# Optimization experiments

Measured on AMD Instinct MI355X. Metric: run time of the kernel, lower is better.

The kernel has to match this reference:

```python
import jax, jax.numpy as jnp
import numpy as np

D_MODEL = 1024
NUM_HEADS = 16
HEAD_DIM = D_MODEL // NUM_HEADS  # 64
THETA = 10000.0
B, S = 2, 2048


def setup_inputs() -> dict:
    key = jax.random.key(0)
    k1, k2, k3 = jax.random.split(key, 3)
    sigma_qkv = (2.0 / (D_MODEL + 3 * D_MODEL)) ** 0.5
    sigma_o = (2.0 / (D_MODEL + D_MODEL)) ** 0.5
    x = jax.random.normal(k1, (B, S, D_MODEL), dtype=jnp.float32)
    w_qkv = jax.random.normal(k2, (3 * D_MODEL, D_MODEL), dtype=jnp.float32) * sigma_qkv
    w_o = jax.random.normal(k3, (D_MODEL, D_MODEL), dtype=jnp.float32) * sigma_o
    token_positions = jnp.arange(S, dtype=jnp.int32)
    return {"x": x, "w_qkv": w_qkv, "w_o": w_o, "token_positions": token_positions, "mask": 1}


def _rope(t, pos):
    # t: (B, H, S, HEAD_DIM); pos: (S,) int
    ids = jnp.arange(HEAD_DIM // 2, dtype=jnp.float32)
    freqs = pos.astype(jnp.float32)[:, None] * (THETA ** (-2.0 * ids / HEAD_DIM))  # (S, HEAD_DIM/2)
    cos, sin = jnp.cos(freqs), jnp.sin(freqs)
    even, odd = t[..., 0::2], t[..., 1::2]
    r_even = even * cos - odd * sin
    r_odd = odd * cos + even * sin
    # interleave back to original layout
    return jnp.stack([r_even, r_odd], axis=-1).reshape(t.shape)


def reference(x, w_qkv, w_o, token_positions, mask):
    # fused QKV projection: Linear computes x @ W^T with W [out, in]
    qkv = x @ w_qkv.T  # (B, S, 3*D_MODEL)
    q, k, v = jnp.split(qkv, 3, axis=-1)

    def to_heads(t):
        return t.reshape(B, S, NUM_HEADS, HEAD_DIM).transpose(0, 2, 1, 3)  # (B, H, S, Dh)

    q, k, v = to_heads(q), to_heads(k), to_heads(v)
    q = _rope(q, token_positions)
    k = _rope(k, token_positions)

    scores = jnp.einsum('bhqd,bhkd->bhqk', q, k)
    if mask:  # causal: lower-triangular allowed
        causal = jnp.tril(jnp.ones((S, S), dtype=bool))
        scores = jnp.where(causal, scores, -jnp.inf)
    attn = jax.nn.softmax(scores * (HEAD_DIM ** -0.5), axis=-1)
    out = jnp.einsum('bhqk,bhkd->bhqd', attn, v)  # (B, H, S, Dh)
    out = out.transpose(0, 2, 1, 3).reshape(B, S, D_MODEL)
    return out @ w_o.T
```

## Files before the change

### kernel.cpp

```cpp
#include <hip/hip_runtime.h>
#include <hip/hip_bf16.h>
#include <math.h>

typedef __bf16 bf16_t;
typedef __bf16 bf16x8 __attribute__((ext_vector_type(8)));
typedef __bf16 bf16x4 __attribute__((ext_vector_type(4)));
typedef float  f32x4  __attribute__((ext_vector_type(4)));

#define D_MODEL 1024
#define NH      16
#define HD      64
#define BATCH   2
#define SEQ     2048
#define MROWS   (BATCH*SEQ)
#define QKVN    (3*D_MODEL)
#define FA_PAD  72
#define SCALE_LOG2E 0.18033688011112042f

__device__ __forceinline__ void async_cp16(const bf16_t* g, bf16_t* l) {
    __builtin_amdgcn_global_load_lds(
        (const __attribute__((address_space(1))) void*)g,
        (__attribute__((address_space(3))) void*)l,
        16, 0, 0);
}

__global__ void cvt_all(const float* __restrict__ x, const float* __restrict__ wq,
                        const float* __restrict__ wo,
                        bf16_t* __restrict__ xb, bf16_t* __restrict__ wqb,
                        bf16_t* __restrict__ wob) {
    const int nx = MROWS * D_MODEL, nq = QKVN * D_MODEL;
    int i = (blockIdx.x * blockDim.x + threadIdx.x) * 4;
    const float* s; bf16_t* d; int off;
    if (i < nx)           { s = x;  d = xb;  off = i; }
    else if (i < nx + nq) { s = wq; d = wqb; off = i - nx; }
    else                  { s = wo; d = wob; off = i - nx - nq; }
    float4 v = *(const float4*)(s + off);
    d[off]     = (bf16_t)v.x;
    d[off + 1] = (bf16_t)v.y;
    d[off + 2] = (bf16_t)v.z;
    d[off + 3] = (bf16_t)v.w;
}

template <typename OutT, int NI>
__global__ __launch_bounds__(256) void gemm_nt(const bf16_t* __restrict__ A,
                                               const bf16_t* __restrict__ Bm,
                                               OutT* __restrict__ C,
                                               int M, int N, int K) {
    __shared__ __align__(16) bf16_t As[128 * 32];
    __shared__ __align__(16) bf16_t Bs[NI * 32 * 32];
    const int tid  = threadIdx.x;
    const int w    = tid >> 6;
    const int lane = tid & 63;
    const int quad = lane >> 4;
    const int l16  = lane & 15;
    const int m0   = blockIdx.x * 128;
    const int n0   = blockIdx.y * (NI * 32);
    const int wm   = (w >> 1) * 64;
    const int wn   = (w & 1) * (NI * 16);

    f32x4 acc[4][NI];
    #pragma unroll
    for (int i = 0; i < 4; i++)
        #pragma unroll
        for (int j = 0; j < NI; j++)
            acc[i][j] = (f32x4){0.f, 0.f, 0.f, 0.f};

    const bf16_t* Ag0 = A  + (size_t)(m0 + (tid >> 2)) * K + (tid & 3) * 8;
    const bf16_t* Ag1 = Ag0 + (size_t)64 * K;
    const bf16_t* Bg0 = Bm + (size_t)(n0 + (tid >> 2)) * K + (tid & 3) * 8;
    const bf16_t* Bg1 = Bg0 + (size_t)64 * K;
    bf16_t* Al0 = &As[(size_t)tid * 8];
    bf16_t* Al1 = &As[((size_t)tid + 256) * 8];
    bf16_t* Bl0 = &Bs[(size_t)tid * 8];
    bf16_t* Bl1 = &Bs[((size_t)tid + 256) * 8];

    for (int k0 = 0; k0 < K; k0 += 32) {
        async_cp16(Ag0 + k0, Al0);
        async_cp16(Ag1 + k0, Al1);
        async_cp16(Bg0 + k0, Bl0);
        if (NI == 4) async_cp16(Bg1 + k0, Bl1);
        __syncthreads();

        bf16x8 af[4], bfr[NI];
        #pragma unroll
        for (int mi = 0; mi < 4; mi++)
            af[mi] = *(const bf16x8*)&As[(wm + mi * 16 + l16) * 32 + quad * 8];
        #pragma unroll
        for (int ni = 0; ni < NI; ni++)
            bfr[ni] = *(const bf16x8*)&Bs[(wn + ni * 16 + l16) * 32 + quad * 8];
        #pragma unroll
        for (int mi = 0; mi < 4; mi++)
            #pragma unroll
            for (int ni = 0; ni < NI; ni++)
                acc[mi][ni] = __builtin_amdgcn_mfma_f32_16x16x32_bf16(
                    af[mi], bfr[ni], acc[mi][ni], 0, 0, 0);
        __syncthreads();
    }

    #pragma unroll
    for (int mi = 0; mi < 4; mi++)
        #pragma unroll
        for (int ni = 0; ni < NI; ni++) {
            const int col = n0 + wn + ni * 16 + l16;
            #pragma unroll
            for (int r = 0; r < 4; r++) {
                const int row = m0 + wm + mi * 16 + quad * 4 + r;
                C[(size_t)row * N + col] = (OutT)acc[mi][ni][r];
            }
        }
}

__global__ __launch_bounds__(256) void rope_split(const bf16_t* __restrict__ qkv,
                                                  const int* __restrict__ pos,
                                                  bf16_t* __restrict__ Qh,
                                                  bf16_t* __restrict__ Kh,
                                                  bf16_t* __restrict__ VT) {
    __shared__ bf16_t vs[128][FA_PAD];
    const int tid   = threadIdx.x;
    const int s_loc = tid >> 1;
    const int half  = tid & 1;
    const int s0    = blockIdx.x * 128;
    const int bh    = blockIdx.y;
    const int b     = bh >> 4, h = bh & 15;
    const int s     = s0 + s_loc;

    const bf16_t* row = qkv + (size_t)(b * SEQ + s) * QKVN + h * HD + half * 32;

    bf16_t qbuf[32], kbuf[32], vbuf[32];
    #pragma unroll
    for (int j = 0; j < 4; j++) {
        *(bf16x8*)&qbuf[j * 8] = *(const bf16x8*)(row + j * 8);
        *(bf16x8*)&kbuf[j * 8] = *(const bf16x8*)(row + D_MODEL + j * 8);
        *(bf16x8*)&vbuf[j * 8] = *(const bf16x8*)(row + 2 * D_MODEL + j * 8);
    }

    const float pf = (float)pos[s];
    #pragma unroll
    for (int p = 0; p < 16; p++) {
        const int d2 = half * 16 + p;
        const float inv = __expf(-0.28782313662425575f * (float)d2);
        const float f = pf * inv;
        const float c = cosf(f), sn = sinf(f);
        float qe = (float)qbuf[2 * p], qo = (float)qbuf[2 * p + 1];
        float ke = (float)kbuf[2 * p], ko = (float)kbuf[2 * p + 1];
        qbuf[2 * p]     = (bf16_t)(qe * c - qo * sn);
        qbuf[2 * p + 1] = (bf16_t)(qo * c + qe * sn);
        kbuf[2 * p]     = (bf16_t)(ke * c - ko * sn);
        kbuf[2 * p + 1] = (bf16_t)(ko * c + ke * sn);
    }

    bf16_t* qdst = Qh + ((size_t)bh * SEQ + s) * HD + half * 32;
    bf16_t* kdst = Kh + ((size_t)bh * SEQ + s) * HD + half * 32;
    #pragma unroll
    for (int j = 0; j < 4; j++) {
        *(bf16x8*)(qdst + j * 8) = *(bf16x8*)&qbuf[j * 8];
        *(bf16x8*)(kdst + j * 8) = *(bf16x8*)&kbuf[j * 8];
        *(bf16x8*)&vs[s_loc][half * 32 + j * 8] = *(bf16x8*)&vbuf[j * 8];
    }
    __syncthreads();

    const int d  = tid >> 2;
    const int sc = tid & 3;
    bf16_t tmp[32];
    #pragma unroll
    for (int i = 0; i < 32; i++) tmp[i] = vs[sc * 32 + i][d];
    bf16_t* vdst = VT + ((size_t)bh * HD + d) * SEQ + s0 + sc * 32;
    #pragma unroll
    for (int j = 0; j < 4; j++)
        *(bf16x8*)(vdst + j * 8) = *(bf16x8*)&tmp[j * 8];
}

__global__ __launch_bounds__(256) void flash_attn(const bf16_t* __restrict__ Qh,
                                                  const bf16_t* __restrict__ Kh,
                                                  const bf16_t* __restrict__ VT,
                                                  bf16_t* __restrict__ AO) {
    __shared__ __align__(16) bf16_t Ks[64 * FA_PAD];
    __shared__ __align__(16) bf16_t Vs[64 * FA_PAD];
    __shared__ __align__(16) bf16_t pT[4][16][FA_PAD];

    const int tid  = threadIdx.x;
    const int w    = tid >> 6;
    const int lane = tid & 63;
    const int quad = lane >> 4;
    const int l16  = lane & 15;

    const int bid = blockIdx.x;
    const int xcd = bid & 7;
    const int mm  = bid >> 3;
    const int bh  = (mm >> 5) * 8 + xcd;
    const int qt  = 31 - (mm & 31);

    const bf16_t* Qb = Qh + (size_t)bh * SEQ * HD;
    const bf16_t* Kb = Kh + (size_t)bh * SEQ * HD;
    const bf16_t* Vb = VT + (size_t)bh * HD * SEQ;

    const int q0 = qt * 64 + w * 16;
    const bf16x8 aq0 = *(const bf16x8*)(Qb + (size_t)(q0 + l16) * HD + quad * 8);
    const bf16x8 aq1 = *(const bf16x8*)(Qb + (size_t)(q0 + l16) * HD + 32 + quad * 8);

    const int srow0 = tid >> 3, scol = (tid & 7) * 8;
    const int lds_off0 = srow0 * FA_PAD + scol;
    const int lds_off1 = (srow0 + 32) * FA_PAD + scol;

    f32x4 o[4];
    #pragma unroll
    for (int i = 0; i < 4; i++) o[i] = (f32x4){0.f, 0.f, 0.f, 0.f};
    float lsum = 0.f;

    bf16x8 sK0 = *(const bf16x8*)(Kb + (size_t)srow0 * HD + scol);
    bf16x8 sK1 = *(const bf16x8*)(Kb + (size_t)(srow0 + 32) * HD + scol);
    bf16x8 sV0 = *(const bf16x8*)(Vb + (size_t)srow0 * SEQ + scol);
    bf16x8 sV1 = *(const bf16x8*)(Vb + (size_t)(srow0 + 32) * SEQ + scol);

    for (int kt = 0; kt <= qt; ++kt) {
        const int k0 = kt * 64;
        __syncthreads();
        *(bf16x8*)&Ks[lds_off0] = sK0;
        *(bf16x8*)&Ks[lds_off1] = sK1;
        *(bf16x8*)&Vs[lds_off0] = sV0;
        *(bf16x8*)&Vs[lds_off1] = sV1;
        __syncthreads();

        bf16x8 nK0, nK1, nV0, nV1;
        if (kt < qt) {
            const int kn = k0 + 64;
            nK0 = *(const bf16x8*)(Kb + (size_t)(kn + srow0) * HD + scol);
            nK1 = *(const bf16x8*)(Kb + (size_t)(kn + srow0 + 32) * HD + scol);
            nV0 = *(const bf16x8*)(Vb + (size_t)srow0 * SEQ + kn + scol);
            nV1 = *(const bf16x8*)(Vb + (size_t)(srow0 + 32) * SEQ + kn + scol);
        }

        const bool diag = (kt == qt);
        #pragma unroll
        for (int ni = 0; ni < 4; ni++) {
            if (diag && ni > w) {
                *(bf16x4*)&pT[w][l16][ni * 16 + quad * 4] = (bf16x4){0, 0, 0, 0};
                continue;
            }
            bf16x8 kb0 = *(const bf16x8*)&Ks[(ni * 16 + l16) * FA_PAD + quad * 8];
            bf16x8 kb1 = *(const bf16x8*)&Ks[(ni * 16 + l16) * FA_PAD + 32 + quad * 8];
            f32x4 t = (f32x4){0.f, 0.f, 0.f, 0.f};
            t = __builtin_amdgcn_mfma_f32_16x16x32_bf16(kb0, aq0, t, 0, 0, 0);
            t = __builtin_amdgcn_mfma_f32_16x16x32_bf16(kb1, aq1, t, 0, 0, 0);
            bf16x4 pk;
            #pragma unroll
            for (int r = 0; r < 4; r++) {
                float pv = exp2f(t[r] * SCALE_LOG2E);
                if (diag && (ni * 16 + quad * 4 + r > w * 16 + l16)) pv = 0.f;
                lsum += pv;
                pk[r] = (bf16_t)pv;
            }
            *(bf16x4*)&pT[w][l16][ni * 16 + quad * 4] = pk;
        }

        #pragma unroll
        for (int ks = 0; ks < 2; ks++) {
            if (diag && w * 16 + 15 < ks * 32) continue;
            bf16x8 ap = *(const bf16x8*)&pT[w][l16][ks * 32 + quad * 8];
            #pragma unroll
            for (int ni = 0; ni < 4; ni++) {
                bf16x8 vb = *(const bf16x8*)&Vs[(ni * 16 + l16) * FA_PAD + ks * 32 + quad * 8];
                o[ni] = __builtin_amdgcn_mfma_f32_16x16x32_bf16(ap, vb, o[ni], 0, 0, 0);
            }
        }

        sK0 = nK0; sK1 = nK1; sV0 = nV0; sV1 = nV1;
    }

    lsum += __shfl_xor(lsum, 16);
    lsum += __shfl_xor(lsum, 32);
    f32x4 linv;
    #pragma unroll
    for (int r = 0; r < 4; r++)
        linv[r] = 1.0f / __shfl(lsum, quad * 4 + r);

    const int b = bh >> 4, h = bh & 15;
    #pragma unroll
    for (int ni = 0; ni < 4; ni++) {
        #pragma unroll
        for (int r = 0; r < 4; r++) {
            const size_t row = (size_t)b * SEQ + q0 + quad * 4 + r;
            AO[row * D_MODEL + h * HD + ni * 16 + l16] = (bf16_t)(o[ni][r] * linv[r]);
        }
    }
}

extern "C" void kernel_launch(void* const* d_in, const int* in_sizes, int n_in,
                              void* d_out, int out_size, void* d_ws, size_t ws_size,
                              hipStream_t stream) {
    const float* x     = (const float*)d_in[0];
    const float* w_qkv = (const float*)d_in[1];
    const float* w_o   = (const float*)d_in[2];
    const int*   tpos  = (const int*)d_in[3];
    float*       out   = (float*)d_out;

    char* ws = (char*)d_ws;
    bf16_t* xb  = (bf16_t*)(ws);
    bf16_t* wqb = (bf16_t*)(ws + 8388608);
    bf16_t* wob = (bf16_t*)(ws + 14680064);
    bf16_t* qkv = (bf16_t*)(ws + 16777216);
    bf16_t* Qh  = (bf16_t*)(ws + 41943040);
    bf16_t* Kh  = (bf16_t*)(ws + 50331648);
    bf16_t* VT  = (bf16_t*)(ws + 58720256);
    bf16_t* AO  = (bf16_t*)(ws + 67108864);

    cvt_all<<<8192, 256, 0, stream>>>(x, w_qkv, w_o, xb, wqb, wob);

    gemm_nt<bf16_t, 4><<<dim3(32, 24), 256, 0, stream>>>(xb, wqb, qkv, MROWS, QKVN, D_MODEL);

    rope_split<<<dim3(SEQ / 128, BATCH * NH), 256, 0, stream>>>(qkv, tpos, Qh, Kh, VT);

    flash_attn<<<1024, 256, 0, stream>>>(Qh, Kh, VT, AO);

    gemm_nt<float, 2><<<dim3(32, 16), 256, 0, stream>>>(AO, wob, out, MROWS, D_MODEL, D_MODEL);
}
```

Baseline: 221.0 us.

## Pair causal query tiles in 512-thread blocks with double-buffered shared K/V

Each 512-thread block now handles two query tiles, a long one (31-pair) and a short one (pair), so every block does the same total causal work and shares its K/V loads between both groups of waves. K/V tiles are double-buffered in LDS, which removes one barrier per iteration by writing the next tile into the other buffer after compute. The aim is to balance load across blocks and cut redundant K/V traffic. The cost is that waves working the short tile idle at barriers once their work is done, and the larger blocks use more LDS and registers.

```diff
diff --git a/kernel.cpp b/kernel.cpp
--- a/kernel.cpp
+++ b/kernel.cpp
@@ -170,101 +170,104 @@
         *(bf16x8*)(vdst + j * 8) = *(bf16x8*)&tmp[j * 8];
 }
 
-__global__ __launch_bounds__(256) void flash_attn(const bf16_t* __restrict__ Qh,
+__global__ __launch_bounds__(512) void flash_attn(const bf16_t* __restrict__ Qh,
                                                   const bf16_t* __restrict__ Kh,
                                                   const bf16_t* __restrict__ VT,
                                                   bf16_t* __restrict__ AO) {
-    __shared__ __align__(16) bf16_t Ks[64 * FA_PAD];
-    __shared__ __align__(16) bf16_t Vs[64 * FA_PAD];
-    __shared__ __align__(16) bf16_t pT[4][16][FA_PAD];
+    __shared__ __align__(16) bf16_t Ks[2][64 * FA_PAD];
+    __shared__ __align__(16) bf16_t Vs[2][64 * FA_PAD];
+    __shared__ __align__(16) bf16_t pT[8][16][FA_PAD];
 
     const int tid  = threadIdx.x;
     const int w    = tid >> 6;
     const int lane = tid & 63;
     const int quad = lane >> 4;
     const int l16  = lane & 15;
-
-    const int bid = blockIdx.x;
-    const int xcd = bid & 7;
-    const int mm  = bid >> 3;
-    const int bh  = (mm >> 5) * 8 + xcd;
-    const int qt  = 31 - (mm & 31);
+    const int wq   = w & 3;
+    const int g    = w >> 2;
+
+    const int bid  = blockIdx.x;
+    const int xcd  = bid & 7;
+    const int mm   = bid >> 3;
+    const int bh   = (mm >> 4) * 8 + xcd;
+    const int pair = mm & 15;
+    const int qt_big = 31 - pair;
+    const int my_qt  = g ? pair : qt_big;
+    const int niter  = qt_big + 1;
 
     const bf16_t* Qb = Qh + (size_t)bh * SEQ * HD;
     const bf16_t* Kb = Kh + (size_t)bh * SEQ * HD;
     const bf16_t* Vb = VT + (size_t)bh * HD * SEQ;
 
-    const int q0 = qt * 64 + w * 16;
+    const int q0 = my_qt * 64 + wq * 16;
     const bf16x8 aq0 = *(const bf16x8*)(Qb + (size_t)(q0 + l16) * HD + quad * 8);
     const bf16x8 aq1 = *(const bf16x8*)(Qb + (size_t)(q0 + l16) * HD + 32 + quad * 8);
 
-    const int srow0 = tid >> 3, scol = (tid & 7) * 8;
-    const int lds_off0 = srow0 * FA_PAD + scol;
-    const int lds_off1 = (srow0 + 32) * FA_PAD + scol;
+    const int srow = tid >> 3, scol = (tid & 7) * 8;
+    const int lds_off = srow * FA_PAD + scol;
 
     f32x4 o[4];
     #pragma unroll
     for (int i = 0; i < 4; i++) o[i] = (f32x4){0.f, 0.f, 0.f, 0.f};
     float lsum = 0.f;
 
-    bf16x8 sK0 = *(const bf16x8*)(Kb + (size_t)srow0 * HD + scol);
-    bf16x8 sK1 = *(const bf16x8*)(Kb + (size_t)(srow0 + 32) * HD + scol);
-    bf16x8 sV0 = *(const bf16x8*)(Vb + (size_t)srow0 * SEQ + scol);
-    bf16x8 sV1 = *(const bf16x8*)(Vb + (size_t)(srow0 + 32) * SEQ + scol);
-
-    for (int kt = 0; kt <= qt; ++kt) {
-        const int k0 = kt * 64;
+    bf16x8 pK = *(const bf16x8*)(Kb + (size_t)srow * HD + scol);
+    bf16x8 pV = *(const bf16x8*)(Vb + (size_t)srow * SEQ + scol);
+    *(bf16x8*)&Ks[0][lds_off] = pK;
+    *(bf16x8*)&Vs[0][lds_off] = pV;
+
+    for (int kt = 0; kt < niter; ++kt) {
+        const int cur = kt & 1;
+        if (kt + 1 < niter) {
+            const int kn = (kt + 1) * 64;
+            pK = *(const bf16x8*)(Kb + (size_t)(kn + srow) * HD + scol);
+            pV = *(const bf16x8*)(Vb + (size_t)srow * SEQ + kn + scol);
+        }
         __syncthreads();
-        *(bf16x8*)&Ks[lds_off0] = sK0;
-        *(bf16x8*)&Ks[lds_off1] = sK1;
-        *(bf16x8*)&Vs[lds_off0] = sV0;
-        *(bf16x8*)&Vs[lds_off1] = sV1;
-        __syncthreads();
-
-        bf16x8 nK0, nK1, nV0, nV1;
-        if (kt < qt) {
-            const int kn = k0 + 64;
-            nK0 = *(const bf16x8*)(Kb + (size_t)(kn + srow0) * HD + scol);
-            nK1 = *(const bf16x8*)(Kb + (size_t)(kn + srow0 + 32) * HD + scol);
-            nV0 = *(const bf16x8*)(Vb + (size_t)srow0 * SEQ + kn + scol);
-            nV1 = *(const bf16x8*)(Vb + (size_t)(srow0 + 32) * SEQ + kn + scol);
-        }
-
-        const bool diag = (kt == qt);
-        #pragma unroll
-        for (int ni = 0; ni < 4; ni++) {
-            if (diag && ni > w) {
-                *(bf16x4*)&pT[w][l16][ni * 16 + quad * 4] = (bf16x4){0, 0, 0, 0};
-                continue;
-            }
-            bf16x8 kb0 = *(const bf16x8*)&Ks[(ni * 16 + l16) * FA_PAD + quad * 8];
-            bf16x8 kb1 = *(const bf16x8*)&Ks[(ni * 16 + l16) * FA_PAD + 32 + quad * 8];
-            f32x4 t = (f32x4){0.f, 0.f, 0.f, 0.f};
-            t = __builtin_amdgcn_mfma_f32_16x16x32_bf16(kb0, aq0, t, 0, 0, 0);
-            t = __builtin_amdgcn_mfma_f32_16x16x32_bf16(kb1, aq1, t, 0, 0, 0);
-            bf16x4 pk;
-            #pragma unroll
-            for (int r = 0; r < 4; r++) {
-                float pv = exp2f(t[r] * SCALE_LOG2E);
-                if (diag && (ni * 16 + quad * 4 + r > w * 16 + l16)) pv = 0.f;
-                lsum += pv;
-                pk[r] = (bf16_t)pv;
-            }
-            *(bf16x4*)&pT[w][l16][ni * 16 + quad * 4] = pk;
-        }
-
-        #pragma unroll
-        for (int ks = 0; ks < 2; ks++) {
-            if (diag && w * 16 + 15 < ks * 32) continue;
-            bf16x8 ap = *(const bf16x8*)&pT[w][l16][ks * 32 + quad * 8];
+
+        if (kt <= my_qt) {
+            const bool diag = (kt == my_qt);
+            const bf16_t* KsC = &Ks[cur][0];
+            const bf16_t* VsC = &Vs[cur][0];
+
             #pragma unroll
             for (int ni = 0; ni < 4; ni++) {
-                bf16x8 vb = *(const bf16x8*)&Vs[(ni * 16 + l16) * FA_PAD + ks * 32 + quad * 8];
-                o[ni] = __builtin_amdgcn_mfma_f32_16x16x32_bf16(ap, vb, o[ni], 0, 0, 0);
+                if (diag && ni > wq) {
+                    *(bf16x4*)&pT[w][l16][ni * 16 + quad * 4] = (bf16x4){0, 0, 0, 0};
+                    continue;
+                }
+                bf16x8 kb0 = *(const bf16x8*)&KsC[(ni * 16 + l16) * FA_PAD + quad * 8];
+                bf16x8 kb1 = *(const bf16x8*)&KsC[(ni * 16 + l16) * FA_PAD + 32 + quad * 8];
+                f32x4 t = (f32x4){0.f, 0.f, 0.f, 0.f};
+                t = __builtin_amdgcn_mfma_f32_16x16x32_bf16(kb0, aq0, t, 0, 0, 0);
+                t = __builtin_amdgcn_mfma_f32_16x16x32_bf16(kb1, aq1, t, 0, 0, 0);
+                bf16x4 pk;
+                #pragma unroll
+                for (int r = 0; r < 4; r++) {
+                    float pv = exp2f(t[r] * SCALE_LOG2E);
+                    if (diag && (ni * 16 + quad * 4 + r > wq * 16 + l16)) pv = 0.f;
+                    lsum += pv;
+                    pk[r] = (bf16_t)pv;
+                }
+                *(bf16x4*)&pT[w][l16][ni * 16 + quad * 4] = pk;
             }
-        }
-
-        sK0 = nK0; sK1 = nK1; sV0 = nV0; sV1 = nV1;
+
+            #pragma unroll
+            for (int ks = 0; ks < 2; ks++) {
+                if (diag && wq * 16 + 15 < ks * 32) continue;
+                bf16x8 ap = *(const bf16x8*)&pT[w][l16][ks * 32 + quad * 8];
+                #pragma unroll
+                for (int ni = 0; ni < 4; ni++) {
+                    bf16x8 vb = *(const bf16x8*)&VsC[(ni * 16 + l16) * FA_PAD + ks * 32 + quad * 8];
+                    o[ni] = __builtin_amdgcn_mfma_f32_16x16x32_bf16(ap, vb, o[ni], 0, 0, 0);
+                }
+            }
+        }
+
+        if (kt + 1 < niter) {
+            *(bf16x8*)&Ks[cur ^ 1][lds_off] = pK;
+            *(bf16x8*)&Vs[cur ^ 1][lds_off] = pV;
+        }
     }
 
     lsum += __shfl_xor(lsum, 16);
@@ -310,7 +313,7 @@
 
     rope_split<<<dim3(SEQ / 128, BATCH * NH), 256, 0, stream>>>(qkv, tpos, Qh, Kh, VT);
 
-    flash_attn<<<1024, 256, 0, stream>>>(Qh, Kh, VT, AO);
+    flash_attn<<<512, 512, 0, stream>>>(Qh, Kh, VT, AO);
 
     gemm_nt<float, 2><<<dim3(32, 16), 256, 0, stream>>>(AO, wob, out, MROWS, D_MODEL, D_MODEL);
 }
```

Result: faster. 201.6 us (-8.8%).
